# Optimization experiments

Measured on AMD Instinct MI355X. Metric: run time of the kernel, lower is better.

## Reference

```python
import jax, jax.numpy as jnp
import numpy as np

SCORER_BIAS = 0.0
LN_EPS = 1e-5


def setup_inputs() -> dict:
    key = jax.random.key(0)
    k0, k1, k2 = jax.random.split(key, 3)
    B, L, D, H = 8, 8192, 1024, 256
    features = jax.random.normal(k0, (B, L, D), dtype=jnp.float32)
    gamma = jnp.ones((D,), jnp.float32)
    beta = jnp.zeros((D,), jnp.float32)
    W1 = (jax.random.normal(k1, (D, H)) * (1.0 / np.sqrt(D))).astype(jnp.float32)
    b1 = jnp.zeros((H,), jnp.float32)
    W2 = (jax.random.normal(k2, (H, 1)) * (1.0 / np.sqrt(H))).astype(jnp.float32)
    b2 = jnp.zeros((1,), jnp.float32)
    return {"features": features, "gamma": gamma, "beta": beta,
            "W1": W1, "b1": b1, "W2": W2, "b2": b2, "k": 512}


def reference(features, gamma, beta, W1, b1, W2, b2, k):
    # LayerNorm over last dim D
    mu = jnp.mean(features, axis=-1, keepdims=True)
    var = jnp.mean(jnp.square(features - mu), axis=-1, keepdims=True)
    x = (features - mu) * jax.lax.rsqrt(var + LN_EPS) * gamma + beta  # [B,L,D]
    # small MLP scorer: Linear -> GELU(exact, matches torch default) -> Linear
    h = jax.nn.gelu(jnp.einsum('bld,dh->blh', x, W1) + b1, approximate=False)
    scores = (jnp.einsum('blh,ho->blo', h, W2) + b2)[..., 0] + SCORER_BIAS  # [B,L]
    # per-row top-k (torch.topk semantics: largest, sorted)
    _, idx = jax.lax.top_k(scores, k)  # [B,k] int32
    # batched gather of original (un-normalized) features
    selected = jnp.take_along_axis(features, idx[..., None], axis=1)  # [B,k,D]
    return selected, scores, idx
```

## Files before the change

kernel.cpp:

```cpp
#include <hip/hip_runtime.h>
#include <math.h>

#define Dk 1024
#define Hk 256
#define Lk 8192
#define Bk 8
#define MTOT (Bk*Lk)

typedef _Float16 f16;
typedef __attribute__((ext_vector_type(8))) _Float16 f16x8;
typedef __attribute__((ext_vector_type(4))) _Float16 f16x4;
typedef __attribute__((ext_vector_type(16))) float f32x16;
typedef unsigned long long u64;

#define BSTEP 16384
#define AR 20
#define APL (128*AR)
#define ABUF (4*APL)

#define GLD_LDS16(g, l)                                                        \
  __builtin_amdgcn_global_load_lds(                                            \
      (const __attribute__((address_space(1))) unsigned int*)(g),              \
      (__attribute__((address_space(3))) unsigned int*)(l), 16, 0, 0)

__global__ __launch_bounds__(1024) void prep_split(
    const float* __restrict__ W1, const float* __restrict__ gamma,
    const float* __restrict__ beta, f16* __restrict__ W1F,
    float* __restrict__ Spart, float* __restrict__ Tpart) {
  __shared__ float ps[1024], pt[1024];
  const int b = blockIdx.x, t = threadIdx.x;
  float sa = 0.f, ta = 0.f;
  #pragma unroll
  for (int j = 0; j < 4; ++j) {
    int idx = j * 65536 + b * 1024 + t;
    int d = idx >> 8, h = idx & 255;
    float w = W1[idx];
    float g = gamma[d];
    sa = fmaf(g, w, sa);
    ta = fmaf(beta[d], w, ta);
    float wg = g * w;
    f16 whi = (f16)wg;
    f16 wlp = (f16)((wg - (float)whi) * 2048.f);
    int s = d >> 5, kc = (d >> 4) & 1, kh = (d >> 3) & 1, kk = d & 7;
    int cb = h >> 5, c = h & 31;
    size_t base = (size_t)s * BSTEP + ((size_t)kc * 8 + cb) * 512
                + (kh * 32 + c) * 8 + kk;
    W1F[base] = whi;
    W1F[base + 8192] = wlp;
  }
  ps[t] = sa; pt[t] = ta;
  __syncthreads();
  if (t < 256) {
    Spart[b * 256 + t] = ps[t] + ps[t + 256] + ps[t + 512] + ps[t + 768];
    Tpart[b * 256 + t] = pt[t] + pt[t + 256] + pt[t + 512] + pt[t + 768];
  }
}

__global__ __launch_bounds__(256) void prep_combine(
    const float* __restrict__ Spart, const float* __restrict__ Tpart,
    const float* __restrict__ b1, float* __restrict__ S, float* __restrict__ Tb) {
  int j = threadIdx.x;
  float s = 0.f, t = 0.f;
  for (int b = 0; b < 64; ++b) { s += Spart[b * 256 + j]; t += Tpart[b * 256 + j]; }
  S[j] = s;
  Tb[j] = t + b1[j];
}

#define MM3(aA, aB, ah, ax, wh, wl)                                            \
  aA = __builtin_amdgcn_mfma_f32_32x32x16_f16(ah, wh, aA, 0, 0, 0);            \
  aB = __builtin_amdgcn_mfma_f32_32x32x16_f16(ah, wl, aB, 0, 0, 0);            \
  aB = __builtin_amdgcn_mfma_f32_32x32x16_f16(ax, wh, aB, 0, 0, 0);

__global__ __launch_bounds__(1024) void scores_mfma(
    const float* __restrict__ F, const f16* __restrict__ W1F,
    const float* __restrict__ S, const float* __restrict__ Tb,
    const float* __restrict__ W2, const float* __restrict__ b2,
    float* __restrict__ scores_out) {
  __shared__ __align__(16) f16 As[2][ABUF];
  __shared__ __align__(16) f16 Bs[2][BSTEP];
  __shared__ float smu[128], srs[128];
  __shared__ float sred[128][4];

  const int tid = threadIdx.x;
  const int RM = blockIdx.x * 128;
  const int w = tid >> 6, lane = tid & 63;
  const int rg = w & 3;
  const int cg = w >> 2;
  const int c31 = lane & 31, kh = lane >> 5;

  const int arow = tid >> 3, kq = tid & 7;
  const int akc = kq >> 2, akoff = (kq & 3) * 4;
  const int aw0 = (akc * 128 + arow) * AR + akoff;
  const float* Aptr = F + (size_t)(RM + arow) * Dk + kq * 4;

  const int ar0 = (rg * 32 + c31) * AR + kh * 8;
  const int br0 = (cg * 2) * 512 + lane * 8;

  f32x16 accA[2], accB[2];
  accA[0] = (f32x16)(0.f); accB[0] = (f32x16)(0.f);
  accA[1] = (f32x16)(0.f); accB[1] = (f32x16)(0.f);

  float rsum = 0.f, rsq = 0.f;

#define SPLIT4(buf, fv)                                                        \
  {                                                                            \
    f16x4 vhi, vlo;                                                            \
    _Pragma("unroll")                                                          \
    for (int e = 0; e < 4; ++e) {                                              \
      float x = (e == 0) ? fv.x : (e == 1) ? fv.y : (e == 2) ? fv.z : fv.w;    \
      rsum += x; rsq = fmaf(x, x, rsq);                                        \
      f16 hi = (f16)x;                                                         \
      vhi[e] = hi;                                                             \
      vlo[e] = (f16)((x - (float)hi) * 2048.f);                                \
    }                                                                          \
    *reinterpret_cast<f16x4*>(&As[buf][aw0])           = vhi;                  \
    *reinterpret_cast<f16x4*>(&As[buf][aw0 + 2 * APL]) = vlo;                  \
  }

  const f16* bsrc = W1F + (size_t)tid * 8;

  GLD_LDS16(bsrc, &Bs[0][tid * 8]);
  GLD_LDS16(bsrc + 8192, &Bs[0][8192 + tid * 8]);
  bsrc += BSTEP;
  float4 av = *reinterpret_cast<const float4*>(Aptr);
  SPLIT4(0, av)
  av = *reinterpret_cast<const float4*>(Aptr + 32);
  __syncthreads();

  for (int s = 0; s < 32; ++s) {
    const int cur = s & 1;
    if (s < 31) {
      GLD_LDS16(bsrc, &Bs[cur ^ 1][tid * 8]);
      GLD_LDS16(bsrc + 8192, &Bs[cur ^ 1][8192 + tid * 8]);
      bsrc += BSTEP;
      SPLIT4(cur ^ 1, av)
      if (s < 30) av = *reinterpret_cast<const float4*>(Aptr + (s + 2) * 32);
    }
    #pragma unroll
    for (int kc = 0; kc < 2; ++kc) {
      const f16* ab = &As[cur][kc * APL + ar0];
      f16x4 h0 = *reinterpret_cast<const f16x4*>(ab);
      f16x4 h1 = *reinterpret_cast<const f16x4*>(ab + 4);
      f16x4 x0 = *reinterpret_cast<const f16x4*>(ab + 2 * APL);
      f16x4 x1 = *reinterpret_cast<const f16x4*>(ab + 2 * APL + 4);
      f16x8 ahi = __builtin_shufflevector(h0, h1, 0, 1, 2, 3, 4, 5, 6, 7);
      f16x8 axl = __builtin_shufflevector(x0, x1, 0, 1, 2, 3, 4, 5, 6, 7);
      #pragma unroll
      for (int nf = 0; nf < 2; ++nf) {
        const f16* bb = &Bs[cur][kc * 4096 + nf * 512 + br0];
        f16x8 wh = *reinterpret_cast<const f16x8*>(bb);
        f16x8 wl = *reinterpret_cast<const f16x8*>(bb + 8192);
        MM3(accA[nf], accB[nf], ahi, axl, wh, wl)
      }
    }
    __syncthreads();
  }

  rsum += __shfl_xor(rsum, 1); rsum += __shfl_xor(rsum, 2); rsum += __shfl_xor(rsum, 4);
  rsq  += __shfl_xor(rsq, 1);  rsq  += __shfl_xor(rsq, 2);  rsq  += __shfl_xor(rsq, 4);
  if ((tid & 7) == 0) {
    float mu  = rsum * (1.f / 1024.f);
    float var = rsq * (1.f / 1024.f) - mu * mu;
    smu[arow] = mu;
    srs[arow] = rsqrtf(var + 1e-5f);
  }
  __syncthreads();

  float s2[2], tb2[2], w2v[2];
  #pragma unroll
  for (int nf = 0; nf < 2; ++nf) {
    int col = cg * 64 + nf * 32 + c31;
    s2[nf] = S[col]; tb2[nf] = Tb[col]; w2v[nf] = W2[col];
  }
  #pragma unroll
  for (int reg = 0; reg < 16; ++reg) {
    const int row = rg * 32 + (reg & 3) + 8 * (reg >> 2) + 4 * kh;
    float mu = smu[row], rs = srs[row];
    float part = 0.f;
    #pragma unroll
    for (int nf = 0; nf < 2; ++nf) {
      float val = accA[nf][reg] + accB[nf][reg] * (1.f / 2048.f);
      float hpre = rs * val - rs * mu * s2[nf] + tb2[nf];
      float g = 0.5f * hpre * (1.f + erff(hpre * 0.70710678118654752f));
      part = fmaf(g, w2v[nf], part);
    }
    part += __shfl_xor(part, 1); part += __shfl_xor(part, 2);
    part += __shfl_xor(part, 4); part += __shfl_xor(part, 8);
    part += __shfl_xor(part, 16);
    if (c31 == 0) sred[row][cg] = part;
  }
  __syncthreads();
  if (tid < 128) {
    float sc = b2[0] + sred[tid][0] + sred[tid][1] + sred[tid][2] + sred[tid][3];
    scores_out[RM + tid] = sc;
  }
}

__global__ __launch_bounds__(512) void topk_stage1(
    const float* __restrict__ scores, u64* __restrict__ kout) {
  __shared__ u64 keys[1024];
  const int blk = blockIdx.x;
  const int batch = blk >> 3, chunk = blk & 7;
  const int t = threadIdx.x;
  #pragma unroll
  for (int j = 0; j < 2; ++j) {
    int i = t + j * 512;
    int gi = chunk * 1024 + i;
    unsigned u = __float_as_uint(scores[(size_t)batch * Lk + gi]);
    unsigned mono = (u & 0x80000000u) ? ~u : (u | 0x80000000u);
    keys[i] = ((u64)(~mono) << 32) | (unsigned)gi;
  }
  __syncthreads();
  for (int size = 2; size <= 1024; size <<= 1) {
    for (int stride = size >> 1; stride > 0; stride >>= 1) {
      int lo = ((t & ~(stride - 1)) << 1) | (t & (stride - 1));
      int hi = lo + stride;
      bool up = ((lo & size) == 0);
      u64 a = keys[lo], c = keys[hi];
      if ((a > c) == up) { keys[lo] = c; keys[hi] = a; }
      __syncthreads();
    }
  }
  kout[(size_t)blk * 512 + t] = keys[t];
}

__global__ __launch_bounds__(512) void topk_stage2(
    const u64* __restrict__ kin, int k,
    float* __restrict__ idx_f, int* __restrict__ idx_i) {
  __shared__ u64 kk[4096];
  __shared__ u64 tmp[2048];
  const int b = blockIdx.x, t = threadIdx.x;
  #pragma unroll
  for (int j = 0; j < 8; ++j) kk[t + j * 512] = kin[(size_t)b * 4096 + t + j * 512];
  __syncthreads();
  #pragma unroll
  for (int j = 0; j < 4; ++j) {
    u64 a = kk[j * 1024 + t];
    u64 c = kk[j * 1024 + 512 + (511 - t)];
    tmp[j * 512 + t] = a < c ? a : c;
  }
  __syncthreads();
  for (int stride = 256; stride > 0; stride >>= 1) {
    #pragma unroll
    for (int w = 0; w < 2; ++w) {
      int p = t + w * 512;
      int r = p >> 8, q = p & 255;
      int lo = r * 512 + (((q & ~(stride - 1)) << 1) | (q & (stride - 1)));
      u64 a = tmp[lo], c = tmp[lo + stride];
      if (a > c) { tmp[lo] = c; tmp[lo + stride] = a; }
    }
    __syncthreads();
  }
  #pragma unroll
  for (int j = 0; j < 2; ++j) {
    u64 a = tmp[j * 1024 + t];
    u64 c = tmp[j * 1024 + 512 + (511 - t)];
    kk[j * 512 + t] = a < c ? a : c;
  }
  __syncthreads();
  for (int stride = 256; stride > 0; stride >>= 1) {
    int r = t >> 8, q = t & 255;
    int lo = r * 512 + (((q & ~(stride - 1)) << 1) | (q & (stride - 1)));
    u64 a = kk[lo], c = kk[lo + stride];
    if (a > c) { kk[lo] = c; kk[lo + stride] = a; }
    __syncthreads();
  }
  {
    u64 a = kk[t];
    u64 c = kk[512 + (511 - t)];
    tmp[t] = a < c ? a : c;
  }
  __syncthreads();
  for (int stride = 256; stride > 0; stride >>= 1) {
    if (t < 256) {
      int lo = ((t & ~(stride - 1)) << 1) | (t & (stride - 1));
      u64 a = tmp[lo], c = tmp[lo + stride];
      if (a > c) { tmp[lo] = c; tmp[lo + stride] = a; }
    }
    __syncthreads();
  }
  if (t < k) {
    int id = (int)(tmp[t] & 0xFFFFFFFFu);
    idx_f[(size_t)b * k + t] = (float)id;
    idx_i[(size_t)b * k + t] = id;
  }
}

__global__ __launch_bounds__(256) void gather_kernel(
    const float* __restrict__ F, const int* __restrict__ idx,
    float* __restrict__ out, int k) {
  int row = blockIdx.x;
  int b = row / k;
  int id = idx[row];
  const float4* src = reinterpret_cast<const float4*>(F + ((size_t)b * Lk + id) * Dk);
  float4* dst = reinterpret_cast<float4*>(out + (size_t)row * Dk);
  dst[threadIdx.x] = src[threadIdx.x];
}

extern "C" void kernel_launch(void* const* d_in, const int* in_sizes, int n_in,
                              void* d_out, int out_size, void* d_ws, size_t ws_size,
                              hipStream_t stream) {
  const float* F     = (const float*)d_in[0];
  const float* gamma = (const float*)d_in[1];
  const float* beta  = (const float*)d_in[2];
  const float* W1    = (const float*)d_in[3];
  const float* b1    = (const float*)d_in[4];
  const float* W2    = (const float*)d_in[5];
  const float* b2    = (const float*)d_in[6];
  int k = (out_size - Bk * Lk) / (Bk * Dk + Bk);

  float* out_sel = (float*)d_out;
  float* out_sc  = out_sel + (size_t)Bk * k * Dk;
  float* out_idx = out_sc + (size_t)Bk * Lk;

  f16*   W1F   = (f16*)d_ws;
  u64*   kout  = (u64*)((char*)d_ws + (1 << 20));
  float* Spart = (float*)((char*)kout + 262144);
  float* Tpart = Spart + 16384;
  float* Sp    = Tpart + 16384;
  float* Tbp   = Sp + Hk;
  int*   idxi  = (int*)(Tbp + Hk);

  hipLaunchKernelGGL(prep_split,   dim3(64),         dim3(1024), 0, stream,
                     W1, gamma, beta, W1F, Spart, Tpart);
  hipLaunchKernelGGL(prep_combine, dim3(1),          dim3(Hk),   0, stream,
                     Spart, Tpart, b1, Sp, Tbp);
  hipLaunchKernelGGL(scores_mfma,  dim3(MTOT / 128), dim3(1024), 0, stream,
                     F, W1F, Sp, Tbp, W2, b2, out_sc);
  hipLaunchKernelGGL(topk_stage1,  dim3(64),         dim3(512),  0, stream,
                     out_sc, kout);
  hipLaunchKernelGGL(topk_stage2,  dim3(Bk),         dim3(512),  0, stream,
                     kout, k, out_idx, idxi);
  hipLaunchKernelGGL(gather_kernel, dim3(Bk * k),    dim3(256),  0, stream,
                     F, idxi, out_sel, k);
}
```

Before: 162.2 us.

## Triple-buffer W1 LDS tiles with partial vmcnt waits instead of full syncs

Moves the W1 tile staging from a double buffer to a triple buffer and issues async global-to-LDS loads two steps ahead. The per-step __syncthreads is replaced by an s_waitcnt vmcnt(3) plus a raw barrier, so loads for the next tile stay in flight across the barrier. The goal is to hide W1 load latency behind the MFMA work. In exchange it uses more LDS, which may lower occupancy. The vmcnt count must also match the in-flight loads, including the A-tile float4 load, or the barrier will not cover the right data. The last iterations issue dummy loads to keep that count uniform.

```diff
diff --git a/kernel.cpp b/kernel.cpp
--- a/kernel.cpp
+++ b/kernel.cpp
@@ -77,7 +77,7 @@
     const float* __restrict__ W2, const float* __restrict__ b2,
     float* __restrict__ scores_out) {
   __shared__ __align__(16) f16 As[2][ABUF];
-  __shared__ __align__(16) f16 Bs[2][BSTEP];
+  __shared__ __align__(16) f16 Bs[3][BSTEP];
   __shared__ float smu[128], srs[128];
   __shared__ float sred[128][4];
 
@@ -117,25 +117,32 @@
     *reinterpret_cast<f16x4*>(&As[buf][aw0 + 2 * APL]) = vlo;                  \
   }
 
-  const f16* bsrc = W1F + (size_t)tid * 8;
-
-  GLD_LDS16(bsrc, &Bs[0][tid * 8]);
-  GLD_LDS16(bsrc + 8192, &Bs[0][8192 + tid * 8]);
-  bsrc += BSTEP;
+#define STEP_BARRIER()                                                         \
+  asm volatile("s_waitcnt vmcnt(3) lgkmcnt(0)" ::: "memory");                  \
+  __builtin_amdgcn_s_barrier();                                                \
+  asm volatile("" ::: "memory");
+
+  GLD_LDS16(W1F + (size_t)tid * 8, &Bs[0][tid * 8]);
+  GLD_LDS16(W1F + (size_t)(1024 + tid) * 8, &Bs[0][8192 + tid * 8]);
+  GLD_LDS16(W1F + BSTEP + (size_t)tid * 8, &Bs[1][tid * 8]);
+  GLD_LDS16(W1F + BSTEP + (size_t)(1024 + tid) * 8, &Bs[1][8192 + tid * 8]);
   float4 av = *reinterpret_cast<const float4*>(Aptr);
   SPLIT4(0, av)
   av = *reinterpret_cast<const float4*>(Aptr + 32);
-  __syncthreads();
+  asm volatile("s_waitcnt vmcnt(3) lgkmcnt(0)" ::: "memory");
+  __builtin_amdgcn_s_barrier();
+  asm volatile("" ::: "memory");
 
   for (int s = 0; s < 32; ++s) {
     const int cur = s & 1;
-    if (s < 31) {
-      GLD_LDS16(bsrc, &Bs[cur ^ 1][tid * 8]);
-      GLD_LDS16(bsrc + 8192, &Bs[cur ^ 1][8192 + tid * 8]);
-      bsrc += BSTEP;
-      SPLIT4(cur ^ 1, av)
-      if (s < 30) av = *reinterpret_cast<const float4*>(Aptr + (s + 2) * 32);
-    }
+    const int bcur = s % 3, bnxt = (s + 2) % 3;
+    {
+      const f16* bsrc = W1F + (size_t)((s + 2) < 32 ? (s + 2) : 0) * BSTEP;
+      GLD_LDS16(bsrc + (size_t)tid * 8, &Bs[bnxt][tid * 8]);
+      GLD_LDS16(bsrc + (size_t)(1024 + tid) * 8, &Bs[bnxt][8192 + tid * 8]);
+    }
+    if (s < 31) SPLIT4(cur ^ 1, av)
+    av = *reinterpret_cast<const float4*>(s < 30 ? Aptr + (s + 2) * 32 : Aptr);
     #pragma unroll
     for (int kc = 0; kc < 2; ++kc) {
       const f16* ab = &As[cur][kc * APL + ar0];
@@ -147,14 +154,16 @@
       f16x8 axl = __builtin_shufflevector(x0, x1, 0, 1, 2, 3, 4, 5, 6, 7);
       #pragma unroll
       for (int nf = 0; nf < 2; ++nf) {
-        const f16* bb = &Bs[cur][kc * 4096 + nf * 512 + br0];
+        const f16* bb = &Bs[bcur][kc * 4096 + nf * 512 + br0];
         f16x8 wh = *reinterpret_cast<const f16x8*>(bb);
         f16x8 wl = *reinterpret_cast<const f16x8*>(bb + 8192);
         MM3(accA[nf], accB[nf], ahi, axl, wh, wl)
       }
     }
-    __syncthreads();
-  }
+    STEP_BARRIER()
+  }
+
+  __syncthreads();
 
   rsum += __shfl_xor(rsum, 1); rsum += __shfl_xor(rsum, 2); rsum += __shfl_xor(rsum, 4);
   rsq  += __shfl_xor(rsq, 1);  rsq  += __shfl_xor(rsq, 2);  rsq  += __shfl_xor(rsq, 4);
```

After: 169.1 us. 1.04x slower.
